# Kernel tuning notes

Hardware: AMD Instinct MI355X
Metric: run time of the kernel (lower is better)

Reference implementation:

```python
import jax, jax.numpy as jnp
import numpy as np

N = 50000      # nodes
E = 800000     # edges (before self-loops)
IN = 128       # in_channels
HID = 32       # hidden_channels per head
H = 4          # in_head
OUT = 40       # out_channels
OH = 1         # out_head
NEG = 0.2      # GATConv default negative_slope
EPS = 1e-5     # BatchNorm eps
SKIP = 0.5     # skip_coefficient


def setup_inputs() -> dict:
    key = jax.random.key(0)
    ks = jax.random.split(key, 24)
    s = 0.1
    f32 = jnp.float32
    return dict(
        x=jax.random.normal(ks[0], (N, IN), dtype=f32),
        W0=jax.random.normal(ks[1], (H * HID, IN), dtype=f32) * s,
        as0=jax.random.normal(ks[2], (H, HID), dtype=f32) * s,
        ad0=jax.random.normal(ks[3], (H, HID), dtype=f32) * s,
        b0=jnp.zeros((H * HID,), f32),
        g0=jnp.ones((H * HID,), f32),
        be0=jnp.zeros((H * HID,), f32),
        W1=jax.random.normal(ks[4], (H * HID, H * HID), dtype=f32) * s,
        as1=jax.random.normal(ks[5], (H, HID), dtype=f32) * s,
        ad1=jax.random.normal(ks[6], (H, HID), dtype=f32) * s,
        b1=jnp.zeros((H * HID,), f32),
        g1=jnp.ones((H * HID,), f32),
        be1=jnp.zeros((H * HID,), f32),
        W2=jax.random.normal(ks[7], (OH * OUT, H * HID), dtype=f32) * s,
        as2=jax.random.normal(ks[8], (OH, OUT), dtype=f32) * s,
        ad2=jax.random.normal(ks[9], (OH, OUT), dtype=f32) * s,
        b2=jnp.zeros((OH * OUT,), f32),
        edge_index=jax.random.randint(ks[10], (2, E), 0, N, dtype=jnp.int64),
    )


def gat_layer(x, src, dst, W, a_s, a_d, b, heads, ch):
    # PyG GATConv (concat=True): per-head linear, edge LeakyReLU attention,
    # softmax over incoming edges per destination node, scatter-add aggregate.
    n = x.shape[0]
    h = (x @ W.T).reshape(n, heads, ch)            # [N,H,C]
    al_s = jnp.einsum('nhc,hc->nh', h, a_s)        # [N,H]
    al_d = jnp.einsum('nhc,hc->nh', h, a_d)
    e = jax.nn.leaky_relu(al_s[src] + al_d[dst], NEG)   # [Etot,H]
    m = jax.ops.segment_max(e, dst, num_segments=n)     # per-dst max (stable softmax)
    ex = jnp.exp(e - m[dst])
    denom = jax.ops.segment_sum(ex, dst, num_segments=n)
    alpha = ex / denom[dst]                              # [Etot,H]
    out = jax.ops.segment_sum(alpha[:, :, None] * h[src], dst, num_segments=n)
    return out.reshape(n, heads * ch) + b


def batchnorm(x, g, b):
    # BatchNorm1d, batch-statistics form
    mu = x.mean(0)
    var = x.var(0)
    return (x - mu) * jax.lax.rsqrt(var + EPS) * g + b


def reference(x, W0, as0, ad0, b0, g0, be0, W1, as1, ad1, b1, g1, be1,
              W2, as2, ad2, b2, edge_index):
    loops = jnp.arange(N, dtype=edge_index.dtype)   # GATConv add_self_loops=True
    src = jnp.concatenate([edge_index[0], loops])
    dst = jnp.concatenate([edge_index[1], loops])
    h = jax.nn.relu(batchnorm(gat_layer(x, src, dst, W0, as0, ad0, b0, H, HID), g0, be0))
    skip = h
    h = gat_layer(h, src, dst, W1, as1, ad1, b1, H, HID)
    h = jax.nn.relu(batchnorm(h, g1, be1) + SKIP * skip)
    return gat_layer(h, src, dst, W2, as2, ad2, b2, OH, OUT)
```

## Files before the change

### kernel.cpp

```cpp
#include <hip/hip_runtime.h>
#include <hip/hip_bf16.h>
#include <stdint.h>

#define N_NODES 50000
#define N_EDGES 800000
#define TOT_EDGES (N_EDGES + N_NODES)
#define DIM 128
#define NEG 0.2f
#define BN_EPS 1e-5f
#define SKIPC 0.5f
#define NB 196
#define BCAP 6144
#define EPB 2048
#define BINA_BLKS ((N_EDGES + EPB - 1) / EPB)

typedef __attribute__((ext_vector_type(8))) short short8;
typedef __attribute__((ext_vector_type(4))) float f32x4;

__device__ inline float bf2f(__hip_bfloat16 v) { return __bfloat162float(v); }
__device__ inline float u16f(unsigned short u) { return __uint_as_float(((unsigned int)u) << 16); }
__device__ inline unsigned short f2bu(float f) {
    __hip_bfloat16 b = __float2bfloat16(f);
    return *(unsigned short*)&b;
}
__device__ inline void fma8(float* acc, float ex, uint4 u) {
    acc[0] += ex * u16f((unsigned short)(u.x & 0xFFFFu));
    acc[1] += ex * u16f((unsigned short)(u.x >> 16));
    acc[2] += ex * u16f((unsigned short)(u.y & 0xFFFFu));
    acc[3] += ex * u16f((unsigned short)(u.y >> 16));
    acc[4] += ex * u16f((unsigned short)(u.z & 0xFFFFu));
    acc[5] += ex * u16f((unsigned short)(u.z >> 16));
    acc[6] += ex * u16f((unsigned short)(u.w & 0xFFFFu));
    acc[7] += ex * u16f((unsigned short)(u.w >> 16));
}
__device__ inline unsigned int pk2(float a, float b) {
    return (unsigned int)f2bu(a) | ((unsigned int)f2bu(b) << 16);
}

__global__ void zero_out_k(unsigned short* out, int n) {
    int g = blockIdx.x * 256 + threadIdx.x;
    if (g < n) out[g] = 0;
}

__device__ inline void binA_body(int bid, const int* __restrict__ ei,
                                 int* __restrict__ bcnt,
                                 unsigned int* __restrict__ pairs) {
    __shared__ int cnt[NB], base[NB], cur[NB];
    __shared__ int sf;
    int t = threadIdx.x;
    if (t == 0) sf = 0;
    for (int i = t; i < NB; i += 256) cnt[i] = 0;
    __syncthreads();
    if (t < 16 && ei[2 * t + 1] != 0) atomicOr(&sf, 1);
    __syncthreads();
    int f = (sf == 0);
    int b0 = bid * EPB;
    unsigned int pk[8];
    int bk[8];
    #pragma unroll
    for (int j = 0; j < 8; ++j) bk[j] = -1;

    auto handle = [&](int slot, int s, int d) {
        if ((unsigned)d < N_NODES && (unsigned)s < N_NODES) {
            bk[slot] = d >> 8;
            pk[slot] = (unsigned int)s | ((unsigned int)(d & 255) << 16);
            atomicAdd(&cnt[bk[slot]], 1);
        }
    };

    if (f) {
        #pragma unroll
        for (int j = 0; j < 4; ++j) {
            int i0 = b0 + j * 512 + 2 * t;
            if (i0 < N_EDGES) {
                int4 sv = *(const int4*)(ei + 2 * (size_t)i0);
                int4 dv = *(const int4*)(ei + 2 * ((size_t)N_EDGES + i0));
                handle(2 * j, sv.x, dv.x);
                if (i0 + 1 < N_EDGES) handle(2 * j + 1, sv.z, dv.z);
            }
        }
    } else {
        #pragma unroll
        for (int j = 0; j < 8; ++j) {
            int g = b0 + j * 256 + t;
            if (g < N_EDGES) handle(j, ei[g], ei[N_EDGES + g]);
        }
    }
    __syncthreads();
    if (t < NB) {
        int c = cnt[t];
        base[t] = c ? atomicAdd(&bcnt[t], c) : 0;
        cur[t] = 0;
    }
    __syncthreads();
    #pragma unroll
    for (int j = 0; j < 8; ++j) {
        if (bk[j] >= 0) {
            int off = base[bk[j]] + atomicAdd(&cur[bk[j]], 1);
            if (off < BCAP) pairs[(size_t)bk[j] * BCAP + off] = pk[j];
        }
    }
}

struct PrepJobs { const void* src[13]; float* dst[13]; int n[13]; };
__device__ inline void wcvt_body(int bid,
                                 const void* __restrict__ W0,
                                 const void* __restrict__ W1,
                                 const void* __restrict__ W2,
                                 unsigned short* __restrict__ Wb0,
                                 unsigned short* __restrict__ Wb1,
                                 unsigned short* __restrict__ Wb2,
                                 const PrepJobs& jobs,
                                 int* __restrict__ fflag) {
    __shared__ int cs;
    int t = threadIdx.x;
    if (t == 0) cs = 0;
    __syncthreads();
    {
        unsigned int w = ((const unsigned int*)W0)[t];
        float v0 = u16f((unsigned short)(w & 0xFFFFu));
        float a = fabsf(v0);
        int sane = (a < 2.0f && (a > 1e-20f || v0 == 0.0f)) ? 1 : 0;
        atomicAdd(&cs, sane);
    }
    __syncthreads();
    int f = (cs >= 128) ? 1 : 0;
    if (bid == 0 && t == 0) fflag[0] = f;
    if (bid < 148) {
        int g = bid * 256 + t;
        const void* W; unsigned short* Wb; int idx;
        if (g < 16384)        { W = W0; Wb = Wb0; idx = g; }
        else if (g < 32768)   { W = W1; Wb = Wb1; idx = g - 16384; }
        else if (g < 37888)   { W = W2; Wb = Wb2; idx = g - 32768; }
        else return;
        if (f) Wb[idx] = ((const unsigned short*)W)[idx];
        else   Wb[idx] = f2bu(((const float*)W)[idx]);
    } else {
        int j = bid - 148;
        int n = jobs.n[j];
        const void* s = jobs.src[j];
        float* d = jobs.dst[j];
        for (int i = t; i < n; i += 256)
            d[i] = f ? bf2f(((const __hip_bfloat16*)s)[i]) : ((const float*)s)[i];
    }
}

__global__ __launch_bounds__(256) void fat1_k(const int* __restrict__ ei,
                                              int* __restrict__ bcnt,
                                              unsigned int* __restrict__ pairs,
                                              const void* __restrict__ W0,
                                              const void* __restrict__ W1,
                                              const void* __restrict__ W2,
                                              unsigned short* __restrict__ Wb0,
                                              unsigned short* __restrict__ Wb1,
                                              unsigned short* __restrict__ Wb2,
                                              PrepJobs jobs,
                                              int* __restrict__ fflag) {
    if (blockIdx.x < BINA_BLKS) binA_body(blockIdx.x, ei, bcnt, pairs);
    else wcvt_body(blockIdx.x - BINA_BLKS, W0, W1, W2, Wb0, Wb1, Wb2, jobs, fflag);
}

__device__ inline void binB_body(int b, const int* __restrict__ bcnt,
                                 const unsigned int* __restrict__ pairs,
                                 int* __restrict__ row_ptr,
                                 int* __restrict__ ssrc) {
    __shared__ int cntL[256], scanL[256], curL[256];
    __shared__ int sred[256];
    int t = threadIdx.x;
    int n0 = b * 256;
    int nn = min(256, N_NODES - n0);
    int cnt_b = min(bcnt[b], BCAP);
    int contrib = 0;
    if (t < b) contrib = min(bcnt[t], BCAP) + min(256, N_NODES - t * 256);
    sred[t] = contrib;
    __syncthreads();
    #pragma unroll
    for (int off = 128; off > 0; off >>= 1) {
        if (t < off) sred[t] += sred[t + off];
        __syncthreads();
    }
    int gbase = sred[0];
    if (b == NB - 1 && t == 0) row_ptr[N_NODES] = gbase + cnt_b + nn;

    const unsigned int* P = pairs + (size_t)b * BCAP;
    cntL[t] = (t < nn) ? 1 : 0;
    __syncthreads();
    for (int i = t; i < cnt_b; i += 256)
        atomicAdd(&cntL[P[i] >> 16], 1);
    __syncthreads();
    int v = cntL[t];
    scanL[t] = v;
    __syncthreads();
    for (int off = 1; off < 256; off <<= 1) {
        int x = (t >= off) ? scanL[t - off] : 0;
        __syncthreads();
        scanL[t] += x;
        __syncthreads();
    }
    int excl = scanL[t] - v;
    if (t < nn) row_ptr[n0 + t] = gbase + excl;
    curL[t] = excl;
    __syncthreads();
    if (t < nn) {
        int pos = atomicAdd(&curL[t], 1);
        ssrc[gbase + pos] = n0 + t;
    }
    for (int i = t; i < cnt_b; i += 256) {
        unsigned int p = P[i];
        int pos = atomicAdd(&curL[p >> 16], 1);
        ssrc[gbase + pos] = (int)(p & 0xFFFFu);
    }
}

__device__ inline void wext_body(int bid,
                                 unsigned short* __restrict__ Wb0,
                                 unsigned short* __restrict__ Wb1,
                                 unsigned short* __restrict__ Wb2,
                                 const float* __restrict__ pAs0, const float* __restrict__ pAd0,
                                 const float* __restrict__ pAs1, const float* __restrict__ pAd1,
                                 const float* __restrict__ pAs2, const float* __restrict__ pAd2) {
    int g = bid * 256 + threadIdx.x;
    if (g < 2048) {
        int layer = g >> 10;
        int gi = g & 1023;
        int rowq = gi >> 7;
        int k = gi & 127;
        int hh = rowq & 3, dir = rowq >> 2;
        unsigned short* Wb = layer ? Wb1 : Wb0;
        const float* p = layer ? (dir ? pAd1 : pAs1) : (dir ? pAd0 : pAs0);
        float v = 0.f;
        #pragma unroll
        for (int c = 0; c < 32; ++c)
            v += p[hh * 32 + c] * u16f(Wb[(size_t)(hh * 32 + c) * 128 + k]);
        Wb[(size_t)(128 + dir * 4 + hh) * 128 + k] = f2bu(v);
    } else if (g < 2304) {
        int gi = g - 2048;
        int dir = gi >> 7;
        int k = gi & 127;
        const float* p = dir ? pAd2 : pAs2;
        float v = 0.f;
        #pragma unroll
        for (int c = 0; c < 40; ++c)
            v += p[c] * u16f(Wb2[(size_t)c * 128 + k]);
        Wb2[(size_t)(40 + dir) * 128 + k] = f2bu(v);
    }
}

__global__ __launch_bounds__(256) void fat2_k(const int* __restrict__ bcnt,
                                              const unsigned int* __restrict__ pairs,
                                              int* __restrict__ row_ptr,
                                              int* __restrict__ ssrc,
                                              unsigned short* __restrict__ Wb0,
                                              unsigned short* __restrict__ Wb1,
                                              unsigned short* __restrict__ Wb2,
                                              const float* __restrict__ pAs0, const float* __restrict__ pAd0,
                                              const float* __restrict__ pAs1, const float* __restrict__ pAd1,
                                              const float* __restrict__ pAs2, const float* __restrict__ pAd2) {
    if (blockIdx.x < NB) binB_body(blockIdx.x, bcnt, pairs, row_ptr, ssrc);
    else wext_body(blockIdx.x - NB, Wb0, Wb1, Wb2, pAs0, pAd0, pAs1, pAd1, pAs2, pAd2);
}

template<int MT, int MV, int ALBASE, int NH, int AMODE>
__device__ inline void mfma_body(const void* __restrict__ X,
                                 const unsigned short* __restrict__ Xprev,
                                 const unsigned short* __restrict__ Wb,
                                 unsigned short* __restrict__ Y,
                                 float* __restrict__ als, float* __restrict__ ald, int n,
                                 const float* __restrict__ bnA, const float* __restrict__ gA,
                                 const float* __restrict__ beA,
                                 const float* __restrict__ bnB, const float* __restrict__ gB,
                                 const float* __restrict__ beB) {
    const int MROWS = ALBASE + 2 * NH;
    __shared__ float sAsc[128], sAsh[128], sBsc[128], sBsh[128];
    if (AMODE >= 2) {
        int t = threadIdx.x;
        const float invN = 1.f / (float)N_NODES;
        if (t < 128) {
            float mean = bnA[t] * invN;
            float var = fmaxf(bnA[128 + t] * invN - mean * mean, 0.f);
            float s = rsqrtf(var + BN_EPS) * gA[t];
            sAsc[t] = s;
            sAsh[t] = beA[t] - mean * s;
        } else if (AMODE == 3) {
            int c = t - 128;
            float mean = bnB[c] * invN;
            float var = fmaxf(bnB[128 + c] * invN - mean * mean, 0.f);
            float s = rsqrtf(var + BN_EPS) * gB[c];
            sBsc[c] = s;
            sBsh[c] = beB[c] - mean * s;
        }
        __syncthreads();
    }
    int wave = (blockIdx.x * blockDim.x + threadIdx.x) >> 6;
    int r0 = wave * 16;
    if (r0 >= n) return;
    int lane = threadIdx.x & 63;
    int m = lane & 15, quad = lane >> 4;
    f32x4 acc[MT];
    #pragma unroll
    for (int t = 0; t < MT; ++t) acc[t] = (f32x4){0.f, 0.f, 0.f, 0.f};
    int arow = min(r0 + m, n - 1);

    #pragma unroll
    for (int kc = 0; kc < 4; ++kc) {
        int k0 = kc * 32 + quad * 8;
        short8 a;
        if (AMODE == 0) {
            const float* xp = (const float*)X + (size_t)arow * 128 + k0;
            float4 x0 = *(const float4*)xp;
            float4 x1 = *(const float4*)(xp + 4);
            a[0] = (short)f2bu(x0.x); a[1] = (short)f2bu(x0.y);
            a[2] = (short)f2bu(x0.z); a[3] = (short)f2bu(x0.w);
            a[4] = (short)f2bu(x1.x); a[5] = (short)f2bu(x1.y);
            a[6] = (short)f2bu(x1.z); a[7] = (short)f2bu(x1.w);
        } else if (AMODE == 1) {
            a = *(const short8*)((const unsigned short*)X + (size_t)arow * 128 + k0);
        } else if (AMODE == 2) {
            short8 hv = *(const short8*)((const unsigned short*)X + (size_t)arow * 128 + k0);
            #pragma unroll
            for (int j = 0; j < 8; ++j) {
                float v = u16f((unsigned short)hv[j]) * sAsc[k0 + j] + sAsh[k0 + j];
                a[j] = (short)f2bu(fmaxf(v, 0.f));
            }
        } else {
            short8 hv = *(const short8*)((const unsigned short*)X + (size_t)arow * 128 + k0);
            short8 pv = *(const short8*)(Xprev + (size_t)arow * 128 + k0);
            #pragma unroll
            for (int j = 0; j < 8; ++j) {
                float v0 = fmaxf(u16f((unsigned short)pv[j]) * sBsc[k0 + j] + sBsh[k0 + j], 0.f);
                float v = u16f((unsigned short)hv[j]) * sAsc[k0 + j] + sAsh[k0 + j] + SKIPC * v0;
                a[j] = (short)f2bu(fmaxf(v, 0.f));
            }
        }
        #pragma unroll
        for (int t = 0; t < MT; ++t) {
            int col = t * 16 + m;
            short8 b;
            if (col < MROWS) b = *(const short8*)(Wb + (size_t)col * 128 + k0);
            else             b = (short8){0,0,0,0,0,0,0,0};
            acc[t] = __builtin_amdgcn_mfma_f32_16x16x32_bf16(a, b, acc[t], 0, 0, 0);
        }
    }

    #pragma unroll
    for (int t = 0; t < MT; ++t) {
        int col = t * 16 + m;
        #pragma unroll
        for (int r = 0; r < 4; ++r) {
            int row = r0 + quad * 4 + r;
            if (row >= n) continue;
            if (col < MV) {
                Y[(size_t)row * MV + col] = f2bu(acc[t][r]);
            } else if (col < ALBASE + NH) {
                als[row * NH + (col - ALBASE)] = acc[t][r];
            } else if (col < ALBASE + 2 * NH) {
                ald[row * NH + (col - ALBASE - NH)] = acc[t][r];
            }
        }
    }
}

__global__ __launch_bounds__(256) void mfma_x_k(const void* __restrict__ X,
                                                const unsigned short* __restrict__ Wb,
                                                unsigned short* __restrict__ Y,
                                                float* __restrict__ als, float* __restrict__ ald,
                                                int n, const int* __restrict__ fflag) {
    if (fflag[0]) mfma_body<9, 128, 128, 4, 1>(X, nullptr, Wb, Y, als, ald, n,
                                               nullptr, nullptr, nullptr, nullptr, nullptr, nullptr);
    else          mfma_body<9, 128, 128, 4, 0>(X, nullptr, Wb, Y, als, ald, n,
                                               nullptr, nullptr, nullptr, nullptr, nullptr, nullptr);
}

__global__ __launch_bounds__(256) void mfma_aff_k(const unsigned short* __restrict__ X,
                                                  const unsigned short* __restrict__ Wb,
                                                  unsigned short* __restrict__ Y,
                                                  float* __restrict__ als, float* __restrict__ ald,
                                                  int n,
                                                  const float* __restrict__ bn,
                                                  const float* __restrict__ g,
                                                  const float* __restrict__ be) {
    mfma_body<9, 128, 128, 4, 2>(X, nullptr, Wb, Y, als, ald, n,
                                 bn, g, be, nullptr, nullptr, nullptr);
}

__global__ __launch_bounds__(256) void mfma_affskip_k(const unsigned short* __restrict__ X,
                                                      const unsigned short* __restrict__ Xprev,
                                                      const unsigned short* __restrict__ Wb,
                                                      unsigned short* __restrict__ Y,
                                                      float* __restrict__ als, float* __restrict__ ald,
                                                      int n,
                                                      const float* __restrict__ bnA,
                                                      const float* __restrict__ gA,
                                                      const float* __restrict__ beA,
                                                      const float* __restrict__ bnB,
                                                      const float* __restrict__ gB,
                                                      const float* __restrict__ beB) {
    mfma_body<3, 40, 40, 1, 3>(X, Xprev, Wb, Y, als, ald, n,
                               bnA, gA, beA, bnB, gB, beB);
}

template<int H, int C, int LPG, int CPL, bool FINAL>
__global__ __launch_bounds__(256) void agg4_k(const unsigned short* __restrict__ hbuf,
                                              const float* __restrict__ als,
                                              const float* __restrict__ ald,
                                              const float* __restrict__ bias,
                                              const int* __restrict__ row_ptr,
                                              const int* __restrict__ ssrc,
                                              void* __restrict__ out,
                                              const int* __restrict__ fflag, int n) {
    const int HC = H * C;
    const int G = 64 / LPG;
    const int NV = CPL / 8;
    int gw = (blockIdx.x * blockDim.x + threadIdx.x) >> 6;
    if (gw >= n) return;
    int lane = threadIdx.x & 63;
    int grp = lane / LPG;
    int sl  = lane % LPG;
    int c0 = sl * CPL;
    bool act = c0 < HC;
    int hl = act ? (c0 / C) : 0;
    int d = gw;
    int beg = row_ptr[d], end = row_ptr[d + 1];
    float adh = ald[d * H + hl];

    float denom = 0.f;
    float acc[CPL];
    #pragma unroll
    for (int j = 0; j < CPL; ++j) acc[j] = 0.f;

    int i0 = beg + grp;
    bool h0 = i0 < end;
    bool h1 = (i0 + G) < end;
    bool h2 = (i0 + 2 * G) < end;
    float al0 = 0.f, al1 = 0.f, al2 = 0.f;
    uint4 u0[NV], u1[NV], u2[NV];
    if (h0) {
        int s = ssrc[i0];
        al0 = als[s * H + hl];
        if (act) {
            const uint4* hp = (const uint4*)(hbuf + (size_t)s * HC + c0);
            #pragma unroll
            for (int v = 0; v < NV; ++v) u0[v] = hp[v];
        }
    }
    if (h1) {
        int s = ssrc[i0 + G];
        al1 = als[s * H + hl];
        if (act) {
            const uint4* hp = (const uint4*)(hbuf + (size_t)s * HC + c0);
            #pragma unroll
            for (int v = 0; v < NV; ++v) u1[v] = hp[v];
        }
    }
    if (h2) {
        int s = ssrc[i0 + 2 * G];
        al2 = als[s * H + hl];
        if (act) {
            const uint4* hp = (const uint4*)(hbuf + (size_t)s * HC + c0);
            #pragma unroll
            for (int v = 0; v < NV; ++v) u2[v] = hp[v];
        }
    }
    int inext = i0 + 3 * G;

    while (h0) {
        bool h3 = inext < end;
        float al3 = 0.f;
        uint4 u3[NV];
        if (h3) {
            int s = ssrc[inext];
            al3 = als[s * H + hl];
            if (act) {
                const uint4* hp = (const uint4*)(hbuf + (size_t)s * HC + c0);
                #pragma unroll
                for (int v = 0; v < NV; ++v) u3[v] = hp[v];
            }
        }
        float t = al0 + adh;
        t = t > 0.f ? t : NEG * t;
        float ex = __expf(t);
        denom += ex;
        if (act) {
            #pragma unroll
            for (int v = 0; v < NV; ++v) fma8(acc + v * 8, ex, u0[v]);
        }
        h0 = h1; al0 = al1;
        #pragma unroll
        for (int v = 0; v < NV; ++v) u0[v] = u1[v];
        h1 = h2; al1 = al2;
        #pragma unroll
        for (int v = 0; v < NV; ++v) u1[v] = u2[v];
        h2 = h3; al2 = al3;
        #pragma unroll
        for (int v = 0; v < NV; ++v) u2[v] = u3[v];
        inext += G;
    }

    #pragma unroll
    for (int off = LPG; off < 64; off <<= 1) {
        denom += __shfl_xor(denom, off, 64);
        #pragma unroll
        for (int j = 0; j < CPL; ++j) acc[j] += __shfl_xor(acc[j], off, 64);
    }

    if (grp == 0 && act) {
        float inv = 1.f / denom;
        float vals[CPL];
        #pragma unroll
        for (int j = 0; j < CPL; ++j) vals[j] = acc[j] * inv + bias[c0 + j];
        if (FINAL && !fflag[0]) {
            float* of = (float*)out + (size_t)d * HC + c0;
            #pragma unroll
            for (int j = 0; j < CPL; ++j) of[j] = vals[j];
        } else {
            unsigned short* ob = (unsigned short*)out + (size_t)d * HC + c0;
            #pragma unroll
            for (int v = 0; v < NV; ++v) {
                uint4 pk;
                pk.x = pk2(vals[v * 8 + 0], vals[v * 8 + 1]);
                pk.y = pk2(vals[v * 8 + 2], vals[v * 8 + 3]);
                pk.z = pk2(vals[v * 8 + 4], vals[v * 8 + 5]);
                pk.w = pk2(vals[v * 8 + 6], vals[v * 8 + 7]);
                *(uint4*)(ob + v * 8) = pk;
            }
        }
    }
}

__global__ __launch_bounds__(256) void bn_stats_k(const unsigned short* __restrict__ x,
                                                  float* __restrict__ sum,
                                                  float* __restrict__ sumsq, int n) {
    __shared__ float ss[128], sq[128];
    int t = threadIdx.x;
    int rt = t >> 4;
    int c8 = (t & 15) * 8;
    float s[8], q[8];
    #pragma unroll
    for (int j = 0; j < 8; ++j) { s[j] = 0.f; q[j] = 0.f; }
    for (int r = blockIdx.x * 16 + rt; r < n; r += gridDim.x * 16) {
        short8 v = *(const short8*)(x + (size_t)r * 128 + c8);
        #pragma unroll
        for (int j = 0; j < 8; ++j) {
            float f = u16f((unsigned short)v[j]);
            s[j] += f; q[j] += f * f;
        }
    }
    if (t < 128) { ss[t] = 0.f; sq[t] = 0.f; }
    __syncthreads();
    #pragma unroll
    for (int j = 0; j < 8; ++j) {
        atomicAdd(&ss[c8 + j], s[j]);
        atomicAdd(&sq[c8 + j], q[j]);
    }
    __syncthreads();
    if (t < 128) {
        atomicAdd(&sum[t], ss[t]);
        atomicAdd(&sumsq[t], sq[t]);
    }
}

extern "C" void kernel_launch(void* const* d_in, const int* in_sizes, int n_in,
                              void* d_out, int out_size, void* d_ws, size_t ws_size,
                              hipStream_t stream) {
    const void* x   = d_in[0];
    const void* W0  = d_in[1];
    const void* as0 = d_in[2];
    const void* ad0 = d_in[3];
    const void* b0  = d_in[4];
    const void* g0  = d_in[5];
    const void* be0 = d_in[6];
    const void* W1  = d_in[7];
    const void* as1 = d_in[8];
    const void* ad1 = d_in[9];
    const void* b1  = d_in[10];
    const void* g1  = d_in[11];
    const void* be1 = d_in[12];
    const void* W2  = d_in[13];
    const void* as2 = d_in[14];
    const void* ad2 = d_in[15];
    const void* b2  = d_in[16];
    const int* ei = (const int*)d_in[17];

    char* w = (char*)d_ws;
    size_t off = 0;
    auto alloc = [&](size_t bytes) -> void* {
        void* p = w + off;
        off = (off + bytes + 255) & ~(size_t)255;
        return p;
    };
    unsigned short* hbf = (unsigned short*)alloc((size_t)N_NODES * 128 * 2);
    unsigned short* hA0 = (unsigned short*)alloc((size_t)N_NODES * 128 * 2);
    unsigned short* hA1 = (unsigned short*)alloc((size_t)N_NODES * 128 * 2);
    float* als = (float*)alloc((size_t)N_NODES * 4 * 4);
    float* ald = (float*)alloc((size_t)N_NODES * 4 * 4);
    unsigned short* Wb0 = (unsigned short*)alloc((size_t)136 * 128 * 2);
    unsigned short* Wb1 = (unsigned short*)alloc((size_t)136 * 128 * 2);
    unsigned short* Wb2 = (unsigned short*)alloc((size_t)42 * 128 * 2);
    float* prm = (float*)alloc(2048 * 4);
    int* zreg = (int*)alloc((size_t)(NB + 512) * 4);
    int* bcnt = zreg;
    float* bn0 = (float*)(zreg + NB);
    float* bn1 = bn0 + 256;
    int* row_ptr = (int*)alloc((size_t)(N_NODES + 1) * 4);
    int* ssrc    = (int*)alloc((size_t)TOT_EDGES * 4);
    unsigned int* pairs = (unsigned int*)alloc((size_t)NB * BCAP * 4);
    int* fflag   = (int*)alloc(256);

    float* pAs0 = prm + 0,   * pAd0 = prm + 128,  * pB0 = prm + 256;
    float* pG0  = prm + 384, * pBe0 = prm + 512;
    float* pAs1 = prm + 640, * pAd1 = prm + 768,  * pB1 = prm + 896;
    float* pG1  = prm + 1024,* pBe1 = prm + 1152;
    float* pAs2 = prm + 1280,* pAd2 = prm + 1320, * pB2 = prm + 1360;

    if (off > ws_size) {
        zero_out_k<<<(out_size + 255) / 256, 256, 0, stream>>>((unsigned short*)d_out, out_size);
        return;
    }

    const int MB = (((N_NODES + 15) / 16) + 3) / 4;
    const int AB = (N_NODES * 64 + 255) / 256;

    PrepJobs jobs;
    const void* srcs[13] = { as0, ad0, b0, g0, be0, as1, ad1, b1, g1, be1, as2, ad2, b2 };
    float* dsts[13] = { pAs0, pAd0, pB0, pG0, pBe0, pAs1, pAd1, pB1, pG1, pBe1, pAs2, pAd2, pB2 };
    int ns[13] = { 128,128,128,128,128, 128,128,128,128,128, 40,40,40 };
    for (int i = 0; i < 13; ++i) { jobs.src[i] = srcs[i]; jobs.dst[i] = dsts[i]; jobs.n[i] = ns[i]; }

    hipMemsetAsync(zreg, 0, (size_t)(NB + 512) * 4, stream);
    fat1_k<<<BINA_BLKS + 161, 256, 0, stream>>>(ei, bcnt, pairs, W0, W1, W2, Wb0, Wb1, Wb2, jobs, fflag);
    fat2_k<<<NB + 9, 256, 0, stream>>>(bcnt, pairs, row_ptr, ssrc, Wb0, Wb1, Wb2,
                                       pAs0, pAd0, pAs1, pAd1, pAs2, pAd2);
    mfma_x_k<<<MB, 256, 0, stream>>>(x, Wb0, hbf, als, ald, N_NODES, fflag);
    agg4_k<4, 32, 8, 16, false><<<AB, 256, 0, stream>>>(hbf, als, ald, pB0, row_ptr, ssrc, hA0, fflag, N_NODES);
    bn_stats_k<<<256, 256, 0, stream>>>(hA0, bn0, bn0 + 128, N_NODES);
    mfma_aff_k<<<MB, 256, 0, stream>>>(hA0, Wb1, hbf, als, ald, N_NODES, bn0, pG0, pBe0);
    agg4_k<4, 32, 8, 16, false><<<AB, 256, 0, stream>>>(hbf, als, ald, pB1, row_ptr, ssrc, hA1, fflag, N_NODES);
    bn_stats_k<<<256, 256, 0, stream>>>(hA1, bn1, bn1 + 128, N_NODES);
    mfma_affskip_k<<<MB, 256, 0, stream>>>(hA1, hA0, Wb2, hbf, als, ald, N_NODES,
                                           bn1, pG1, pBe1, bn0, pG0, pBe0);
    agg4_k<1, 40, 8, 8, true><<<AB, 256, 0, stream>>>(hbf, als, ald, pB2, row_ptr, ssrc, d_out, fflag, N_NODES);
}
```

Baseline: 323.7 us.

## Fuse first-layer GEMM into CSR build kernel and fold weight extension into prep

The attention-vector extension rows of the weights are now computed directly from the raw input weights inside the first prep kernel, with dtype detected locally. The separate weight-extension blocks in the second prep kernel go away. The first GEMM is merged into the CSR-build kernel as extra blocks, which removes one launch and lets binning and GEMM run concurrently. The cost is duplicated dtype detection and a larger heterogeneous grid. There is also a possible race: the GEMM reads Wb0 rows written in the previous kernel, which is fine across launches.

```diff
diff --git a/kernel.cpp b/kernel.cpp
--- a/kernel.cpp
+++ b/kernel.cpp
@@ -13,6 +13,8 @@
 #define BCAP 6144
 #define EPB 2048
 #define BINA_BLKS ((N_EDGES + EPB - 1) / EPB)
+#define GEMM_JOBS ((N_NODES + 63) >> 6)
+#define ZN (NB + 512)
 
 typedef __attribute__((ext_vector_type(8))) short short8;
 typedef __attribute__((ext_vector_type(4))) float f32x4;
@@ -145,19 +147,58 @@
     }
 }
 
-__global__ __launch_bounds__(256) void fat1_k(const int* __restrict__ ei,
-                                              int* __restrict__ bcnt,
-                                              unsigned int* __restrict__ pairs,
-                                              const void* __restrict__ W0,
-                                              const void* __restrict__ W1,
-                                              const void* __restrict__ W2,
-                                              unsigned short* __restrict__ Wb0,
-                                              unsigned short* __restrict__ Wb1,
-                                              unsigned short* __restrict__ Wb2,
-                                              PrepJobs jobs,
-                                              int* __restrict__ fflag) {
-    if (blockIdx.x < BINA_BLKS) binA_body(blockIdx.x, ei, bcnt, pairs);
-    else wcvt_body(blockIdx.x - BINA_BLKS, W0, W1, W2, Wb0, Wb1, Wb2, jobs, fflag);
+__device__ inline void wext_raw_body(int bid,
+                                     const void* __restrict__ W0,
+                                     const void* __restrict__ W1,
+                                     const void* __restrict__ W2,
+                                     const void* __restrict__ as0, const void* __restrict__ ad0,
+                                     const void* __restrict__ as1, const void* __restrict__ ad1,
+                                     const void* __restrict__ as2, const void* __restrict__ ad2,
+                                     unsigned short* __restrict__ Wb0,
+                                     unsigned short* __restrict__ Wb1,
+                                     unsigned short* __restrict__ Wb2) {
+    __shared__ int cs;
+    int t = threadIdx.x;
+    if (t == 0) cs = 0;
+    __syncthreads();
+    {
+        unsigned int w = ((const unsigned int*)W0)[t];
+        float v0 = u16f((unsigned short)(w & 0xFFFFu));
+        float a = fabsf(v0);
+        int sane = (a < 2.0f && (a > 1e-20f || v0 == 0.0f)) ? 1 : 0;
+        atomicAdd(&cs, sane);
+    }
+    __syncthreads();
+    int f = (cs >= 128) ? 1 : 0;
+    auto rd = [&](const void* p, int idx) -> float {
+        return f ? u16f(((const unsigned short*)p)[idx]) : ((const float*)p)[idx];
+    };
+    int g = bid * 256 + t;
+    if (g < 2048) {
+        int layer = g >> 10;
+        int gi = g & 1023;
+        int rowq = gi >> 7;
+        int k = gi & 127;
+        int hh = rowq & 3, dir = rowq >> 2;
+        const void* W = layer ? W1 : W0;
+        const void* p = layer ? (dir ? ad1 : as1) : (dir ? ad0 : as0);
+        unsigned short* Wb = layer ? Wb1 : Wb0;
+        float v = 0.f;
+        #pragma unroll
+        for (int c = 0; c < 32; ++c)
+            v += rd(p, hh * 32 + c) * rd(W, (hh * 32 + c) * 128 + k);
+        Wb[(size_t)(128 + dir * 4 + hh) * 128 + k] = f2bu(v);
+    } else if (g < 2304) {
+        int gi = g - 2048;
+        int dir = gi >> 7;
+        int k = gi & 127;
+        const void* p = dir ? ad2 : as2;
+        float v = 0.f;
+        #pragma unroll
+        for (int c = 0; c < 40; ++c)
+            v += rd(p, c) * rd(W2, c * 128 + k);
+        Wb2[(size_t)(40 + dir) * 128 + k] = f2bu(v);
+    }
 }
 
 __device__ inline void binB_body(int b, const int* __restrict__ bcnt,
@@ -212,64 +253,17 @@
     }
 }
 
-__device__ inline void wext_body(int bid,
-                                 unsigned short* __restrict__ Wb0,
-                                 unsigned short* __restrict__ Wb1,
-                                 unsigned short* __restrict__ Wb2,
-                                 const float* __restrict__ pAs0, const float* __restrict__ pAd0,
-                                 const float* __restrict__ pAs1, const float* __restrict__ pAd1,
-                                 const float* __restrict__ pAs2, const float* __restrict__ pAd2) {
-    int g = bid * 256 + threadIdx.x;
-    if (g < 2048) {
-        int layer = g >> 10;
-        int gi = g & 1023;
-        int rowq = gi >> 7;
-        int k = gi & 127;
-        int hh = rowq & 3, dir = rowq >> 2;
-        unsigned short* Wb = layer ? Wb1 : Wb0;
-        const float* p = layer ? (dir ? pAd1 : pAs1) : (dir ? pAd0 : pAs0);
-        float v = 0.f;
-        #pragma unroll
-        for (int c = 0; c < 32; ++c)
-            v += p[hh * 32 + c] * u16f(Wb[(size_t)(hh * 32 + c) * 128 + k]);
-        Wb[(size_t)(128 + dir * 4 + hh) * 128 + k] = f2bu(v);
-    } else if (g < 2304) {
-        int gi = g - 2048;
-        int dir = gi >> 7;
-        int k = gi & 127;
-        const float* p = dir ? pAd2 : pAs2;
-        float v = 0.f;
-        #pragma unroll
-        for (int c = 0; c < 40; ++c)
-            v += p[c] * u16f(Wb2[(size_t)c * 128 + k]);
-        Wb2[(size_t)(40 + dir) * 128 + k] = f2bu(v);
-    }
-}
-
-__global__ __launch_bounds__(256) void fat2_k(const int* __restrict__ bcnt,
-                                              const unsigned int* __restrict__ pairs,
-                                              int* __restrict__ row_ptr,
-                                              int* __restrict__ ssrc,
-                                              unsigned short* __restrict__ Wb0,
-                                              unsigned short* __restrict__ Wb1,
-                                              unsigned short* __restrict__ Wb2,
-                                              const float* __restrict__ pAs0, const float* __restrict__ pAd0,
-                                              const float* __restrict__ pAs1, const float* __restrict__ pAd1,
-                                              const float* __restrict__ pAs2, const float* __restrict__ pAd2) {
-    if (blockIdx.x < NB) binB_body(blockIdx.x, bcnt, pairs, row_ptr, ssrc);
-    else wext_body(blockIdx.x - NB, Wb0, Wb1, Wb2, pAs0, pAd0, pAs1, pAd1, pAs2, pAd2);
-}
-
 template<int MT, int MV, int ALBASE, int NH, int AMODE>
-__device__ inline void mfma_body(const void* __restrict__ X,
-                                 const unsigned short* __restrict__ Xprev,
-                                 const unsigned short* __restrict__ Wb,
-                                 unsigned short* __restrict__ Y,
-                                 float* __restrict__ als, float* __restrict__ ald, int n,
-                                 const float* __restrict__ bnA, const float* __restrict__ gA,
-                                 const float* __restrict__ beA,
-                                 const float* __restrict__ bnB, const float* __restrict__ gB,
-                                 const float* __restrict__ beB) {
+__device__ inline void gemm_job(int job,
+                                const void* __restrict__ X,
+                                const unsigned short* __restrict__ Xprev,
+                                const unsigned short* __restrict__ Wb,
+                                unsigned short* __restrict__ Y,
+                                float* __restrict__ als, float* __restrict__ ald, int n,
+                                const float* __restrict__ bnA, const float* __restrict__ gA,
+                                const float* __restrict__ beA,
+                                const float* __restrict__ bnB, const float* __restrict__ gB,
+                                const float* __restrict__ beB) {
     const int MROWS = ALBASE + 2 * NH;
     __shared__ float sAsc[128], sAsh[128], sBsc[128], sBsh[128];
     if (AMODE >= 2) {
@@ -291,11 +285,11 @@
         }
         __syncthreads();
     }
-    int wave = (blockIdx.x * blockDim.x + threadIdx.x) >> 6;
-    int r0 = wave * 16;
-    if (r0 >= n) return;
     int lane = threadIdx.x & 63;
     int m = lane & 15, quad = lane >> 4;
+    int wl = threadIdx.x >> 6;
+    int r0 = (job << 6) + (wl << 4);
+    if (r0 >= n) return;
     f32x4 acc[MT];
     #pragma unroll
     for (int t = 0; t < MT; ++t) acc[t] = (f32x4){0.f, 0.f, 0.f, 0.f};
@@ -360,15 +354,46 @@
     }
 }
 
-__global__ __launch_bounds__(256) void mfma_x_k(const void* __restrict__ X,
-                                                const unsigned short* __restrict__ Wb,
-                                                unsigned short* __restrict__ Y,
-                                                float* __restrict__ als, float* __restrict__ ald,
-                                                int n, const int* __restrict__ fflag) {
-    if (fflag[0]) mfma_body<9, 128, 128, 4, 1>(X, nullptr, Wb, Y, als, ald, n,
-                                               nullptr, nullptr, nullptr, nullptr, nullptr, nullptr);
-    else          mfma_body<9, 128, 128, 4, 0>(X, nullptr, Wb, Y, als, ald, n,
-                                               nullptr, nullptr, nullptr, nullptr, nullptr, nullptr);
+__global__ __launch_bounds__(256) void fat1_k(const int* __restrict__ ei,
+                                              int* __restrict__ bcnt,
+                                              unsigned int* __restrict__ pairs,
+                                              const void* __restrict__ W0,
+                                              const void* __restrict__ W1,
+                                              const void* __restrict__ W2,
+                                              const void* __restrict__ as0, const void* __restrict__ ad0,
+                                              const void* __restrict__ as1, const void* __restrict__ ad1,
+                                              const void* __restrict__ as2, const void* __restrict__ ad2,
+                                              unsigned short* __restrict__ Wb0,
+                                              unsigned short* __restrict__ Wb1,
+                                              unsigned short* __restrict__ Wb2,
+                                              PrepJobs jobs,
+                                              int* __restrict__ fflag) {
+    if (blockIdx.x < BINA_BLKS) binA_body(blockIdx.x, ei, bcnt, pairs);
+    else if (blockIdx.x < BINA_BLKS + 161)
+        wcvt_body(blockIdx.x - BINA_BLKS, W0, W1, W2, Wb0, Wb1, Wb2, jobs, fflag);
+    else
+        wext_raw_body(blockIdx.x - BINA_BLKS - 161, W0, W1, W2,
+                      as0, ad0, as1, ad1, as2, ad2, Wb0, Wb1, Wb2);
+}
+
+__global__ __launch_bounds__(256) void fat2b_k(const int* __restrict__ bcnt,
+                                               const unsigned int* __restrict__ pairs,
+                                               int* __restrict__ row_ptr,
+                                               int* __restrict__ ssrc,
+                                               const void* __restrict__ X,
+                                               const unsigned short* __restrict__ Wb,
+                                               unsigned short* __restrict__ Y,
+                                               float* __restrict__ als, float* __restrict__ ald,
+                                               int n, const int* __restrict__ fflag) {
+    if (blockIdx.x < NB) {
+        binB_body(blockIdx.x, bcnt, pairs, row_ptr, ssrc);
+    } else {
+        int job = blockIdx.x - NB;
+        if (fflag[0]) gemm_job<9, 128, 128, 4, 1>(job, X, nullptr, Wb, Y, als, ald, n,
+                                                  nullptr, nullptr, nullptr, nullptr, nullptr, nullptr);
+        else          gemm_job<9, 128, 128, 4, 0>(job, X, nullptr, Wb, Y, als, ald, n,
+                                                  nullptr, nullptr, nullptr, nullptr, nullptr, nullptr);
+    }
 }
 
 __global__ __launch_bounds__(256) void mfma_aff_k(const unsigned short* __restrict__ X,
@@ -379,8 +404,8 @@
                                                   const float* __restrict__ bn,
                                                   const float* __restrict__ g,
                                                   const float* __restrict__ be) {
-    mfma_body<9, 128, 128, 4, 2>(X, nullptr, Wb, Y, als, ald, n,
-                                 bn, g, be, nullptr, nullptr, nullptr);
+    gemm_job<9, 128, 128, 4, 2>(blockIdx.x, X, nullptr, Wb, Y, als, ald, n,
+                                bn, g, be, nullptr, nullptr, nullptr);
 }
 
 __global__ __launch_bounds__(256) void mfma_affskip_k(const unsigned short* __restrict__ X,
@@ -395,8 +420,8 @@
                                                       const float* __restrict__ bnB,
                                                       const float* __restrict__ gB,
                                                       const float* __restrict__ beB) {
-    mfma_body<3, 40, 40, 1, 3>(X, Xprev, Wb, Y, als, ald, n,
-                               bnA, gA, beA, bnB, gB, beB);
+    gemm_job<3, 40, 40, 1, 3>(blockIdx.x, X, Xprev, Wb, Y, als, ald, n,
+                              bnA, gA, beA, bnB, gB, beB);
 }
 
 template<int H, int C, int LPG, int CPL, bool FINAL>
@@ -597,7 +622,7 @@
     unsigned short* Wb1 = (unsigned short*)alloc((size_t)136 * 128 * 2);
     unsigned short* Wb2 = (unsigned short*)alloc((size_t)42 * 128 * 2);
     float* prm = (float*)alloc(2048 * 4);
-    int* zreg = (int*)alloc((size_t)(NB + 512) * 4);
+    int* zreg = (int*)alloc((size_t)ZN * 4);
     int* bcnt = zreg;
     float* bn0 = (float*)(zreg + NB);
     float* bn1 = bn0 + 256;
@@ -617,7 +642,6 @@
         return;
     }
 
-    const int MB = (((N_NODES + 15) / 16) + 3) / 4;
     const int AB = (N_NODES * 64 + 255) / 256;
 
     PrepJobs jobs;
@@ -626,17 +650,18 @@
     int ns[13] = { 128,128,128,128,128, 128,128,128,128,128, 40,40,40 };
     for (int i = 0; i < 13; ++i) { jobs.src[i] = srcs[i]; jobs.dst[i] = dsts[i]; jobs.n[i] = ns[i]; }
 
-    hipMemsetAsync(zreg, 0, (size_t)(NB + 512) * 4, stream);
-    fat1_k<<<BINA_BLKS + 161, 256, 0, stream>>>(ei, bcnt, pairs, W0, W1, W2, Wb0, Wb1, Wb2, jobs, fflag);
-    fat2_k<<<NB + 9, 256, 0, stream>>>(bcnt, pairs, row_ptr, ssrc, Wb0, Wb1, Wb2,
-                                       pAs0, pAd0, pAs1, pAd1, pAs2, pAd2);
-    mfma_x_k<<<MB, 256, 0, stream>>>(x, Wb0, hbf, als, ald, N_NODES, fflag);
+    hipMemsetAsync(zreg, 0, (size_t)ZN * 4, stream);
+    fat1_k<<<BINA_BLKS + 161 + 9, 256, 0, stream>>>(ei, bcnt, pairs, W0, W1, W2,
+                                                    as0, ad0, as1, ad1, as2, ad2,
+                                                    Wb0, Wb1, Wb2, jobs, fflag);
+    fat2b_k<<<NB + GEMM_JOBS, 256, 0, stream>>>(bcnt, pairs, row_ptr, ssrc,
+                                                x, Wb0, hbf, als, ald, N_NODES, fflag);
     agg4_k<4, 32, 8, 16, false><<<AB, 256, 0, stream>>>(hbf, als, ald, pB0, row_ptr, ssrc, hA0, fflag, N_NODES);
     bn_stats_k<<<256, 256, 0, stream>>>(hA0, bn0, bn0 + 128, N_NODES);
-    mfma_aff_k<<<MB, 256, 0, stream>>>(hA0, Wb1, hbf, als, ald, N_NODES, bn0, pG0, pBe0);
+    mfma_aff_k<<<GEMM_JOBS, 256, 0, stream>>>(hA0, Wb1, hbf, als, ald, N_NODES, bn0, pG0, pBe0);
     agg4_k<4, 32, 8, 16, false><<<AB, 256, 0, stream>>>(hbf, als, ald, pB1, row_ptr, ssrc, hA1, fflag, N_NODES);
     bn_stats_k<<<256, 256, 0, stream>>>(hA1, bn1, bn1 + 128, N_NODES);
-    mfma_affskip_k<<<MB, 256, 0, stream>>>(hA1, hA0, Wb2, hbf, als, ald, N_NODES,
-                                           bn1, pG1, pBe1, bn0, pG0, pBe0);
+    mfma_affskip_k<<<GEMM_JOBS, 256, 0, stream>>>(hA1, hA0, Wb2, hbf, als, ald, N_NODES,
+                                                  bn1, pG1, pBe1, bn0, pG0, pBe0);
     agg4_k<1, 40, 8, 8, true><<<AB, 256, 0, stream>>>(hbf, als, ald, pB2, row_ptr, ssrc, d_out, fflag, N_NODES);
 }
```

Result: faster. 312.2 us (-3.5%).
